# Kernel tuning notes

Hardware: AMD Instinct MI355X
Metric: run time of the kernel (lower is better)

Reference implementation:

```python
import jax, jax.numpy as jnp
import numpy as np

B, N, K, D, H = 8, 128, 64, 256, 8  # batch, groups, keys-per-query, k_dim (=h_size), n_head


def setup_inputs() -> dict:
    key = jax.random.key(0)
    kq, kk, kv, kw, kb = jax.random.split(key, 5)
    bound = 1.0 / np.sqrt(D)  # torch nn.Bilinear default init bound
    return {
        "q": jax.random.normal(kq, (B, N, 1, D), jnp.float32),
        "k": jax.random.normal(kk, (B, N, K, D), jnp.float32),
        "v": jax.random.normal(kv, (B, N, K, D), jnp.float32),
        "W": jax.random.uniform(kw, (H, D, D), jnp.float32, -bound, bound),
        "b": jax.random.uniform(kb, (H,), jnp.float32, -bound, bound),
    }


def reference(q, k, v, W, b):
    Bs, Ns, Ks, Ds = k.shape
    Hh = W.shape[0]
    qe = q[:, :, 0, :]  # (B,N,D); torch expands q over K, einsum broadcasts instead
    # nn.Bilinear: scores[b,n,k,h] = q[b,n,:] @ W[h] @ k[b,n,k,:] + b[h]
    scores = jnp.einsum('bnd,hde,bnke->bnkh', qe, W, k) + b  # (B,N,K,H)
    # Faithful to torch's .view(B, N, -1, K): row-major reinterpretation of the
    # trailing (K, H) pair as (H, K) — a dim-mixing reshape, not a transpose.
    attn = scores.reshape(Bs, Ns, Hh, Ks)
    attn = jax.nn.softmax(attn, axis=-1)  # softmax over last dim (dropout p=0)
    # matmul(attn, v) -> (B,N,H,Dv); then sum over the head axis
    output = jnp.einsum('bnhk,bnkd->bnd', attn, v)
    return output, attn
```

## Files before the change

### kernel.cpp

```cpp
#include <hip/hip_runtime.h>
#include <math.h>

namespace {

constexpr int D = 256;
constexpr int H = 8;

typedef __attribute__((ext_vector_type(8))) short bf16x8;
typedef __attribute__((ext_vector_type(4))) float f32x4;

__device__ inline unsigned short bf16rn(float x) {
  unsigned u = __builtin_bit_cast(unsigned, x);
  u += 0x7fffu + ((u >> 16) & 1u);
  return (unsigned short)(u >> 16);
}
__device__ inline float bf16tof(unsigned short b) {
  return __builtin_bit_cast(float, (unsigned)b << 16);
}

constexpr size_t OFF_QW  = 0;
constexpr size_t OFF_WFH = (size_t)8 << 20;
constexpr size_t OFF_WFL = (size_t)9 << 20;
constexpr size_t OFF_QFH = (size_t)10 << 20;
constexpr size_t OFF_QFL = ((size_t)10 << 20) + ((size_t)512 << 10);

__global__ __launch_bounds__(256) void prep_kernel(
    const float* __restrict__ q, const float* __restrict__ W,
    char* __restrict__ ws) {
  const int gid = blockIdx.x * 256 + threadIdx.x;
  float e[8];
  char *hi_base, *lo_base;
  size_t outoff;
  if (gid < 65536) {
    const int l = gid & 63, ks = (gid >> 6) & 7, he = gid >> 9;
    const int h = he >> 4, et = he & 15;
    const int d0 = ks * 32 + ((l >> 4) << 3);
    const int ecol = et * 16 + (l & 15);
    const float* src = W + (size_t)h * 65536 + (size_t)d0 * 256 + ecol;
    #pragma unroll
    for (int j = 0; j < 8; ++j) e[j] = src[j * 256];
    hi_base = ws + OFF_WFH; lo_base = ws + OFF_WFL;
    outoff = (size_t)gid * 16;
  } else {
    const int t = gid - 65536;
    const int l = t & 63, ks = (t >> 6) & 7, bt = t >> 9;
    const int row = bt * 16 + (l & 15);
    const int d0 = ks * 32 + ((l >> 4) << 3);
    const float4* src = reinterpret_cast<const float4*>(q + (size_t)row * 256 + d0);
    float4 a = src[0], b = src[1];
    e[0] = a.x; e[1] = a.y; e[2] = a.z; e[3] = a.w;
    e[4] = b.x; e[5] = b.y; e[6] = b.z; e[7] = b.w;
    hi_base = ws + OFF_QFH; lo_base = ws + OFF_QFL;
    outoff = (size_t)t * 16;
  }
  unsigned hw[4], lw[4];
  #pragma unroll
  for (int p = 0; p < 4; ++p) {
    unsigned short h0 = bf16rn(e[2 * p]), h1 = bf16rn(e[2 * p + 1]);
    unsigned short l0 = bf16rn(e[2 * p] - bf16tof(h0));
    unsigned short l1 = bf16rn(e[2 * p + 1] - bf16tof(h1));
    hw[p] = (unsigned)h0 | ((unsigned)h1 << 16);
    lw[p] = (unsigned)l0 | ((unsigned)l1 << 16);
  }
  *reinterpret_cast<uint4*>(hi_base + outoff) = make_uint4(hw[0], hw[1], hw[2], hw[3]);
  *reinterpret_cast<uint4*>(lo_base + outoff) = make_uint4(lw[0], lw[1], lw[2], lw[3]);
}

__global__ __launch_bounds__(256) void qw_mfma_kernel(
    const char* __restrict__ ws_in, float* __restrict__ qW) {
  const int tid = threadIdx.x;
  const int w   = blockIdx.x * 4 + (tid >> 6);
  const int l   = tid & 63;
  const int bng = w >> 5;
  const int heg = w & 31;
  const char* qfh = ws_in + OFF_QFH;
  const char* qfl = ws_in + OFF_QFL;
  const char* wfh = ws_in + OFF_WFH;
  const char* wfl = ws_in + OFF_WFL;

  f32x4 acc[2][4];
  #pragma unroll
  for (int i = 0; i < 2; ++i)
    #pragma unroll
    for (int j = 0; j < 4; ++j) acc[i][j] = {0.f, 0.f, 0.f, 0.f};

  #pragma unroll 2
  for (int ks = 0; ks < 8; ++ks) {
    bf16x8 aH[2], aL[2], bH[4], bL[4];
    #pragma unroll
    for (int i = 0; i < 2; ++i) {
      const size_t off = ((size_t)((bng * 2 + i) * 8 + ks) * 64 + l) * 16;
      aH[i] = *reinterpret_cast<const bf16x8*>(qfh + off);
      aL[i] = *reinterpret_cast<const bf16x8*>(qfl + off);
    }
    #pragma unroll
    for (int j = 0; j < 4; ++j) {
      const size_t off = ((size_t)((heg * 4 + j) * 8 + ks) * 64 + l) * 16;
      bH[j] = *reinterpret_cast<const bf16x8*>(wfh + off);
      bL[j] = *reinterpret_cast<const bf16x8*>(wfl + off);
    }
    #pragma unroll
    for (int i = 0; i < 2; ++i)
      #pragma unroll
      for (int j = 0; j < 4; ++j) {
        acc[i][j] = __builtin_amdgcn_mfma_f32_16x16x32_bf16(aH[i], bH[j], acc[i][j], 0, 0, 0);
        acc[i][j] = __builtin_amdgcn_mfma_f32_16x16x32_bf16(aH[i], bL[j], acc[i][j], 0, 0, 0);
        acc[i][j] = __builtin_amdgcn_mfma_f32_16x16x32_bf16(aL[i], bH[j], acc[i][j], 0, 0, 0);
      }
  }

  const int rbase = (l >> 4) * 4;
  const int col   = l & 15;
  #pragma unroll
  for (int i = 0; i < 2; ++i)
    #pragma unroll
    for (int j = 0; j < 4; ++j) {
      const size_t cidx = (size_t)(heg * 4 + j) * 16 + col;
      #pragma unroll
      for (int r = 0; r < 4; ++r) {
        const int bn = (bng * 2 + i) * 16 + rbase + r;
        qW[(size_t)bn * 2048 + cidx] = acc[i][j][r];
      }
    }
}

constexpr int FB2   = 0;
constexpr int WSP2  = 8320;
constexpr int SMEM3 = 9344;

__global__ __launch_bounds__(256, 4) void attn_fused_kernel(
    const float* __restrict__ qW, const float* __restrict__ kin,
    const float* __restrict__ vin, const float* __restrict__ bin,
    float* __restrict__ out, float* __restrict__ attn_out) {
  __shared__ alignas(16) long long smem_ll[SMEM3 / 8];
  char* sm = reinterpret_cast<char*>(smem_ll);
  float* wsp = reinterpret_cast<float*>(sm + WSP2);
  const int tid = threadIdx.x;
  const int bn  = blockIdx.x;
  const int wid = tid >> 6;
  const int ln  = tid & 63;

  const float* arow = kin + (size_t)bn * 16384 +
                      (size_t)(wid * 16 + (ln & 15)) * 256 + ((ln >> 4) << 3);
  float4 ka[16];
  #pragma unroll
  for (int ks = 0; ks < 8; ++ks) {
    ka[2 * ks]     = *reinterpret_cast<const float4*>(arow + ks * 32);
    ka[2 * ks + 1] = *reinterpret_cast<const float4*>(arow + ks * 32 + 4);
  }
  const float4* qw4 = reinterpret_cast<const float4*>(qW) + (size_t)bn * 512;
  float4 qv0 = qw4[tid];
  float4 qv1 = qw4[tid + 256];

  {
    const int ks = tid >> 5, slot = 32 + (tid & 31);
    *reinterpret_cast<uint4*>(sm + FB2 + ks * 1040 + slot * 16) =
        make_uint4(0u, 0u, 0u, 0u);
  }
  #pragma unroll
  for (int i = 0; i < 2; ++i) {
    int p = tid + 256 * i;
    int hh = p >> 6, equad = p & 63;
    int ks = equad >> 3, g = (equad >> 1) & 3, j0 = (equad & 1) * 4;
    int base = FB2 + ks * 1040 + (hh * 4 + g) * 16 + j0 * 2;
    float4 qv = i == 0 ? qv0 : qv1;
    unsigned short h0 = bf16rn(qv.x), h1 = bf16rn(qv.y),
                   h2 = bf16rn(qv.z), h3 = bf16rn(qv.w);
    *reinterpret_cast<uint2*>(sm + base) =
        make_uint2((unsigned)h0 | ((unsigned)h1 << 16),
                   (unsigned)h2 | ((unsigned)h3 << 16));
  }
  __syncthreads();

  const int slot_r = (ln & 15) * 4 + (ln >> 4);
  const char* pbH = sm + FB2 + slot_r * 16;
  f32x4 acc = {0.f, 0.f, 0.f, 0.f};
  #pragma unroll
  for (int ks = 0; ks < 8; ++ks) {
    const float4 a0 = ka[2 * ks], a1 = ka[2 * ks + 1];
    bf16x8 aH;
    aH[0] = (short)bf16rn(a0.x); aH[1] = (short)bf16rn(a0.y);
    aH[2] = (short)bf16rn(a0.z); aH[3] = (short)bf16rn(a0.w);
    aH[4] = (short)bf16rn(a1.x); aH[5] = (short)bf16rn(a1.y);
    aH[6] = (short)bf16rn(a1.z); aH[7] = (short)bf16rn(a1.w);
    bf16x8 bH = *reinterpret_cast<const bf16x8*>(pbH + ks * 1040);
    acc = __builtin_amdgcn_mfma_f32_16x16x32_bf16(aH, bH, acc, 0, 0, 0);
  }

  const float bias = bin[ln & 7];
  const int col = ln & 15;
  const bool valid = col < 8;
  float x0 = acc[0] + bias, x1 = acc[1] + bias, x2 = acc[2] + bias, x3 = acc[3] + bias;
  float m = valid ? fmaxf(fmaxf(x0, x1), fmaxf(x2, x3)) : -1e30f;
  m = fmaxf(m, __shfl_xor(m, 1, 64));
  m = fmaxf(m, __shfl_xor(m, 2, 64));
  m = fmaxf(m, __shfl_xor(m, 4, 64));
  m = fmaxf(m, __shfl_xor(m, 16, 64));
  float e0 = valid ? expf(x0 - m) : 0.f;
  float e1 = valid ? expf(x1 - m) : 0.f;
  float e2 = valid ? expf(x2 - m) : 0.f;
  float e3 = valid ? expf(x3 - m) : 0.f;
  float s = e0 + e1 + e2 + e3;
  s += __shfl_xor(s, 1, 64);
  s += __shfl_xor(s, 2, 64);
  s += __shfl_xor(s, 4, 64);
  s += __shfl_xor(s, 16, 64);
  float inv = 1.f / s;
  float p0 = e0 * inv, p1 = e1 * inv, p2 = e2 * inv, p3 = e3 * inv;
  if (valid) {
    size_t base = (size_t)bn * 512 + (size_t)(wid * 16 + (ln >> 4) * 4) * 8 + col;
    attn_out[base]      = p0;
    attn_out[base + 8]  = p1;
    attn_out[base + 16] = p2;
    attn_out[base + 24] = p3;
  }
  p0 += __shfl_xor(p0, 32, 64);
  p1 += __shfl_xor(p1, 32, 64);
  p2 += __shfl_xor(p2, 32, 64);
  p3 += __shfl_xor(p3, 32, 64);
  if (ln < 32 && (ln & 15) < 8) {
    const int rb = (ln >> 4) * 4;
    const int c8 = ln & 7;
    float* w = wsp + wid * 64;
    w[(rb + 0) * 8 + c8] = p0;
    w[(rb + 1) * 8 + c8] = p1;
    w[(rb + 2) * 8 + c8] = p2;
    w[(rb + 3) * 8 + c8] = p3;
  }
  __syncthreads();

  const float4* v4 = reinterpret_cast<const float4*>(vin) + (size_t)bn * 4096;
  float4 av = make_float4(0.f, 0.f, 0.f, 0.f);
  #pragma unroll
  for (int i = 0; i < 16; ++i) {
    const int r = wid + 4 * i;
    float w = wsp[r] + wsp[64 + r] + wsp[128 + r] + wsp[192 + r];
    float4 vv = v4[r * 64 + ln];
    av.x += w * vv.x; av.y += w * vv.y; av.z += w * vv.z; av.w += w * vv.w;
  }
  float* s_red = reinterpret_cast<float*>(sm);
  *reinterpret_cast<float4*>(&s_red[wid * 260 + (ln << 2)]) = av;
  __syncthreads();

  out[(size_t)bn * D + tid] =
      s_red[tid] + s_red[260 + tid] + s_red[520 + tid] + s_red[780 + tid];
}

}

extern "C" void kernel_launch(void* const* d_in, const int* in_sizes, int n_in,
                              void* d_out, int out_size, void* d_ws, size_t ws_size,
                              hipStream_t stream) {
  const float* q = (const float*)d_in[0];
  const float* k = (const float*)d_in[1];
  const float* v = (const float*)d_in[2];
  const float* W = (const float*)d_in[3];
  const float* b = (const float*)d_in[4];

  float* out  = (float*)d_out;
  float* attn = out + 262144;
  char*  ws   = (char*)d_ws;
  float* qWbuf = (float*)(ws + OFF_QW);

  hipLaunchKernelGGL(prep_kernel,       dim3(384),  dim3(256), 0, stream, q, W, ws);
  hipLaunchKernelGGL(qw_mfma_kernel,    dim3(256),  dim3(256), 0, stream, ws, qWbuf);
  hipLaunchKernelGGL(attn_fused_kernel, dim3(1024), dim3(256), 0, stream,
                     qWbuf, k, v, b, out, attn);
}
```

Baseline: 42.24 us.

## Map one wave per (b,n) group and drop block-level barriers in attention kernel

The fused attention kernel now gives each wave a whole (b,n) group, with four groups per block, and each wave has its own LDS slice. A wave loops serially over the four 16-key tiles, accumulating softmax weights in registers. This removes every __syncthreads and the cross-wave shared-memory reduction for the output. It also batches the v loads into 16-wide register arrays. The trade-off is a 4x smaller grid with longer serial work per wave, which may hurt memory-latency hiding on this bandwidth-heavy kernel.

```diff
diff --git a/kernel.cpp b/kernel.cpp
--- a/kernel.cpp
+++ b/kernel.cpp
@@ -124,126 +124,129 @@
     }
 }
 
-constexpr int FB2   = 0;
-constexpr int WSP2  = 8320;
-constexpr int SMEM3 = 9344;
-
-__global__ __launch_bounds__(256, 4) void attn_fused_kernel(
+constexpr int WAVE_LDS = 8576;
+
+__global__ __attribute__((amdgpu_waves_per_eu(1, 4))) __launch_bounds__(256)
+void attn_fused_kernel(
     const float* __restrict__ qW, const float* __restrict__ kin,
     const float* __restrict__ vin, const float* __restrict__ bin,
     float* __restrict__ out, float* __restrict__ attn_out) {
-  __shared__ alignas(16) long long smem_ll[SMEM3 / 8];
-  char* sm = reinterpret_cast<char*>(smem_ll);
-  float* wsp = reinterpret_cast<float*>(sm + WSP2);
+  __shared__ alignas(16) char sm_all[4][WAVE_LDS];
   const int tid = threadIdx.x;
-  const int bn  = blockIdx.x;
   const int wid = tid >> 6;
   const int ln  = tid & 63;
-
-  const float* arow = kin + (size_t)bn * 16384 +
-                      (size_t)(wid * 16 + (ln & 15)) * 256 + ((ln >> 4) << 3);
-  float4 ka[16];
-  #pragma unroll
-  for (int ks = 0; ks < 8; ++ks) {
-    ka[2 * ks]     = *reinterpret_cast<const float4*>(arow + ks * 32);
-    ka[2 * ks + 1] = *reinterpret_cast<const float4*>(arow + ks * 32 + 4);
-  }
+  const int bn  = blockIdx.x * 4 + wid;
+  char* sm = sm_all[wid];
+  float* wsum_l = reinterpret_cast<float*>(sm + 8320);
+
   const float4* qw4 = reinterpret_cast<const float4*>(qW) + (size_t)bn * 512;
-  float4 qv0 = qw4[tid];
-  float4 qv1 = qw4[tid + 256];
-
+  float4 qv[8];
+  #pragma unroll
+  for (int i = 0; i < 8; ++i) qv[i] = qw4[i * 64 + ln];
+  #pragma unroll
+  for (int t = 0; t < 4; ++t) {
+    int z = t * 64 + ln;
+    int ks = z >> 5, slot = 32 + (z & 31);
+    *reinterpret_cast<uint4*>(sm + ks * 1040 + slot * 16) = make_uint4(0u, 0u, 0u, 0u);
+  }
   {
-    const int ks = tid >> 5, slot = 32 + (tid & 31);
-    *reinterpret_cast<uint4*>(sm + FB2 + ks * 1040 + slot * 16) =
-        make_uint4(0u, 0u, 0u, 0u);
-  }
-  #pragma unroll
-  for (int i = 0; i < 2; ++i) {
-    int p = tid + 256 * i;
-    int hh = p >> 6, equad = p & 63;
-    int ks = equad >> 3, g = (equad >> 1) & 3, j0 = (equad & 1) * 4;
-    int base = FB2 + ks * 1040 + (hh * 4 + g) * 16 + j0 * 2;
-    float4 qv = i == 0 ? qv0 : qv1;
-    unsigned short h0 = bf16rn(qv.x), h1 = bf16rn(qv.y),
-                   h2 = bf16rn(qv.z), h3 = bf16rn(qv.w);
-    *reinterpret_cast<uint2*>(sm + base) =
-        make_uint2((unsigned)h0 | ((unsigned)h1 << 16),
-                   (unsigned)h2 | ((unsigned)h3 << 16));
-  }
-  __syncthreads();
-
-  const int slot_r = (ln & 15) * 4 + (ln >> 4);
-  const char* pbH = sm + FB2 + slot_r * 16;
-  f32x4 acc = {0.f, 0.f, 0.f, 0.f};
-  #pragma unroll
-  for (int ks = 0; ks < 8; ++ks) {
-    const float4 a0 = ka[2 * ks], a1 = ka[2 * ks + 1];
-    bf16x8 aH;
-    aH[0] = (short)bf16rn(a0.x); aH[1] = (short)bf16rn(a0.y);
-    aH[2] = (short)bf16rn(a0.z); aH[3] = (short)bf16rn(a0.w);
-    aH[4] = (short)bf16rn(a1.x); aH[5] = (short)bf16rn(a1.y);
-    aH[6] = (short)bf16rn(a1.z); aH[7] = (short)bf16rn(a1.w);
-    bf16x8 bH = *reinterpret_cast<const bf16x8*>(pbH + ks * 1040);
-    acc = __builtin_amdgcn_mfma_f32_16x16x32_bf16(aH, bH, acc, 0, 0, 0);
+    const int ks = ln >> 3, g = (ln >> 1) & 3, j0 = (ln & 1) * 4;
+    #pragma unroll
+    for (int i = 0; i < 8; ++i) {
+      int base = ks * 1040 + (i * 4 + g) * 16 + j0 * 2;
+      unsigned short h0 = bf16rn(qv[i].x), h1 = bf16rn(qv[i].y),
+                     h2 = bf16rn(qv[i].z), h3 = bf16rn(qv[i].w);
+      *reinterpret_cast<uint2*>(sm + base) =
+          make_uint2((unsigned)h0 | ((unsigned)h1 << 16),
+                     (unsigned)h2 | ((unsigned)h3 << 16));
+    }
   }
 
   const float bias = bin[ln & 7];
   const int col = ln & 15;
   const bool valid = col < 8;
-  float x0 = acc[0] + bias, x1 = acc[1] + bias, x2 = acc[2] + bias, x3 = acc[3] + bias;
-  float m = valid ? fmaxf(fmaxf(x0, x1), fmaxf(x2, x3)) : -1e30f;
-  m = fmaxf(m, __shfl_xor(m, 1, 64));
-  m = fmaxf(m, __shfl_xor(m, 2, 64));
-  m = fmaxf(m, __shfl_xor(m, 4, 64));
-  m = fmaxf(m, __shfl_xor(m, 16, 64));
-  float e0 = valid ? expf(x0 - m) : 0.f;
-  float e1 = valid ? expf(x1 - m) : 0.f;
-  float e2 = valid ? expf(x2 - m) : 0.f;
-  float e3 = valid ? expf(x3 - m) : 0.f;
-  float s = e0 + e1 + e2 + e3;
-  s += __shfl_xor(s, 1, 64);
-  s += __shfl_xor(s, 2, 64);
-  s += __shfl_xor(s, 4, 64);
-  s += __shfl_xor(s, 16, 64);
-  float inv = 1.f / s;
-  float p0 = e0 * inv, p1 = e1 * inv, p2 = e2 * inv, p3 = e3 * inv;
-  if (valid) {
-    size_t base = (size_t)bn * 512 + (size_t)(wid * 16 + (ln >> 4) * 4) * 8 + col;
-    attn_out[base]      = p0;
-    attn_out[base + 8]  = p1;
-    attn_out[base + 16] = p2;
-    attn_out[base + 24] = p3;
-  }
-  p0 += __shfl_xor(p0, 32, 64);
-  p1 += __shfl_xor(p1, 32, 64);
-  p2 += __shfl_xor(p2, 32, 64);
-  p3 += __shfl_xor(p3, 32, 64);
+  const int slot_r = (ln & 15) * 4 + (ln >> 4);
+  const char* pbH = sm + slot_r * 16;
+  const float* kbase = kin + (size_t)bn * 16384 +
+                       (size_t)(ln & 15) * 256 + ((ln >> 4) << 3);
+
+  float wa0 = 0.f, wa1 = 0.f, wa2 = 0.f, wa3 = 0.f;
+
+  for (int T = 0; T < 4; ++T) {
+    const float* arow = kbase + T * 16 * 256;
+    float4 ka[16];
+    #pragma unroll
+    for (int ks = 0; ks < 8; ++ks) {
+      ka[2 * ks]     = *reinterpret_cast<const float4*>(arow + ks * 32);
+      ka[2 * ks + 1] = *reinterpret_cast<const float4*>(arow + ks * 32 + 4);
+    }
+    f32x4 acc = {0.f, 0.f, 0.f, 0.f};
+    #pragma unroll
+    for (int ks = 0; ks < 8; ++ks) {
+      const float4 a0 = ka[2 * ks], a1 = ka[2 * ks + 1];
+      bf16x8 aH;
+      aH[0] = (short)bf16rn(a0.x); aH[1] = (short)bf16rn(a0.y);
+      aH[2] = (short)bf16rn(a0.z); aH[3] = (short)bf16rn(a0.w);
+      aH[4] = (short)bf16rn(a1.x); aH[5] = (short)bf16rn(a1.y);
+      aH[6] = (short)bf16rn(a1.z); aH[7] = (short)bf16rn(a1.w);
+      bf16x8 bH = *reinterpret_cast<const bf16x8*>(pbH + ks * 1040);
+      acc = __builtin_amdgcn_mfma_f32_16x16x32_bf16(aH, bH, acc, 0, 0, 0);
+    }
+    float x0 = acc[0] + bias, x1 = acc[1] + bias, x2 = acc[2] + bias, x3 = acc[3] + bias;
+    float m = valid ? fmaxf(fmaxf(x0, x1), fmaxf(x2, x3)) : -1e30f;
+    m = fmaxf(m, __shfl_xor(m, 1, 64));
+    m = fmaxf(m, __shfl_xor(m, 2, 64));
+    m = fmaxf(m, __shfl_xor(m, 4, 64));
+    m = fmaxf(m, __shfl_xor(m, 16, 64));
+    float e0 = valid ? expf(x0 - m) : 0.f;
+    float e1 = valid ? expf(x1 - m) : 0.f;
+    float e2 = valid ? expf(x2 - m) : 0.f;
+    float e3 = valid ? expf(x3 - m) : 0.f;
+    float s = e0 + e1 + e2 + e3;
+    s += __shfl_xor(s, 1, 64);
+    s += __shfl_xor(s, 2, 64);
+    s += __shfl_xor(s, 4, 64);
+    s += __shfl_xor(s, 16, 64);
+    float inv = 1.f / s;
+    float p0 = e0 * inv, p1 = e1 * inv, p2 = e2 * inv, p3 = e3 * inv;
+    if (valid) {
+      size_t base = (size_t)bn * 512 + (size_t)(T * 16 + (ln >> 4) * 4) * 8 + col;
+      attn_out[base]      = p0;
+      attn_out[base + 8]  = p1;
+      attn_out[base + 16] = p2;
+      attn_out[base + 24] = p3;
+    }
+    p0 += __shfl_xor(p0, 32, 64);
+    p1 += __shfl_xor(p1, 32, 64);
+    p2 += __shfl_xor(p2, 32, 64);
+    p3 += __shfl_xor(p3, 32, 64);
+    wa0 += p0; wa1 += p1; wa2 += p2; wa3 += p3;
+  }
+
   if (ln < 32 && (ln & 15) < 8) {
     const int rb = (ln >> 4) * 4;
     const int c8 = ln & 7;
-    float* w = wsp + wid * 64;
-    w[(rb + 0) * 8 + c8] = p0;
-    w[(rb + 1) * 8 + c8] = p1;
-    w[(rb + 2) * 8 + c8] = p2;
-    w[(rb + 3) * 8 + c8] = p3;
-  }
-  __syncthreads();
+    wsum_l[(rb + 0) * 8 + c8] = wa0;
+    wsum_l[(rb + 1) * 8 + c8] = wa1;
+    wsum_l[(rb + 2) * 8 + c8] = wa2;
+    wsum_l[(rb + 3) * 8 + c8] = wa3;
+  }
 
   const float4* v4 = reinterpret_cast<const float4*>(vin) + (size_t)bn * 4096;
   float4 av = make_float4(0.f, 0.f, 0.f, 0.f);
   #pragma unroll
-  for (int i = 0; i < 16; ++i) {
-    const int r = wid + 4 * i;
-    float w = wsp[r] + wsp[64 + r] + wsp[128 + r] + wsp[192 + r];
-    float4 vv = v4[r * 64 + ln];
-    av.x += w * vv.x; av.y += w * vv.y; av.z += w * vv.z; av.w += w * vv.w;
-  }
-  float* s_red = reinterpret_cast<float*>(sm);
-  *reinterpret_cast<float4*>(&s_red[wid * 260 + (ln << 2)]) = av;
-  __syncthreads();
-
-  out[(size_t)bn * D + tid] =
-      s_red[tid] + s_red[260 + tid] + s_red[520 + tid] + s_red[780 + tid];
+  for (int rb = 0; rb < 4; ++rb) {
+    float4 vv[16];
+    #pragma unroll
+    for (int i = 0; i < 16; ++i) vv[i] = v4[(size_t)(rb * 16 + i) * 64 + ln];
+    #pragma unroll
+    for (int i = 0; i < 16; ++i) {
+      float w = wsum_l[rb * 16 + i];
+      av.x += w * vv[i].x; av.y += w * vv[i].y;
+      av.z += w * vv[i].z; av.w += w * vv[i].w;
+    }
+  }
+  *reinterpret_cast<float4*>(&out[(size_t)bn * D + ln * 4]) = av;
 }
 
 }
@@ -262,8 +265,8 @@
   char*  ws   = (char*)d_ws;
   float* qWbuf = (float*)(ws + OFF_QW);
 
-  hipLaunchKernelGGL(prep_kernel,       dim3(384),  dim3(256), 0, stream, q, W, ws);
-  hipLaunchKernelGGL(qw_mfma_kernel,    dim3(256),  dim3(256), 0, stream, ws, qWbuf);
-  hipLaunchKernelGGL(attn_fused_kernel, dim3(1024), dim3(256), 0, stream,
+  hipLaunchKernelGGL(prep_kernel,       dim3(384), dim3(256), 0, stream, q, W, ws);
+  hipLaunchKernelGGL(qw_mfma_kernel,    dim3(256), dim3(256), 0, stream, ws, qWbuf);
+  hipLaunchKernelGGL(attn_fused_kernel, dim3(256), dim3(256), 0, stream,
                      qWbuf, k, v, b, out, attn);
 }
```

Result: slower. 48.54 us (+14.9%).
